# Kernel tuning notes

Hardware: AMD Instinct MI355X
Metric: run time of the kernel (lower is better)

The kernel has to match this reference:

```python
import jax, jax.numpy as jnp
import numpy as np

N, IN_SIZE, FEAT, N_OUT = 8192, 512, 128, 512
ALPHA = 0.5


def setup_inputs() -> dict:
    key = jax.random.key(0)
    ks = jax.random.split(key, 5)
    return {
        "x": jax.random.normal(ks[0], (N, IN_SIZE), dtype=jnp.float32),
        "W0": jax.random.normal(ks[1], (FEAT, IN_SIZE), dtype=jnp.float32) * (1.0 / np.sqrt(IN_SIZE)),
        "W1": jax.random.normal(ks[2], (FEAT, IN_SIZE), dtype=jnp.float32) * (1.0 / np.sqrt(IN_SIZE)),
        "weight": jax.random.normal(ks[3], (IN_SIZE, N_OUT), dtype=jnp.float32),
        "weight_time": jax.random.normal(ks[4], (IN_SIZE, N_OUT), dtype=jnp.float32),
    }


def time_affinity(n: int) -> jnp.ndarray:
    # Closed form of the numpy roll/triu/flip construction: M[i,j] = n - |i-j|,
    # then rows normalized to sum to 1.
    idx = jnp.arange(n)
    M = (n - jnp.abs(idx[:, None] - idx[None, :])).astype(jnp.float32)
    return M / jnp.sum(M, axis=1, keepdims=True)


def reference(x, W0, W1, weight, weight_time):
    n = x.shape[0]
    q = x @ W0.T                      # [N, FEAT]
    k = x @ W1.T                      # [N, FEAT]
    G = jax.nn.softmax(q @ k.T, axis=1)   # [N, N] learned affinity
    G_time = time_affinity(n)              # [N, N] static affinity
    out = (G @ x) @ weight                 # [N, N_OUT]
    out_time = (G_time @ x) @ weight_time  # [N, N_OUT]
    return ALPHA * out + (1.0 - ALPHA) * out_time
```

## Files before the change

### kernel.cpp

```cpp
#include <hip/hip_runtime.h>
#include <math.h>

#define NN 8192
#define INS 512
#define FEAT 128

typedef unsigned short ush;
typedef short bf16x8 __attribute__((ext_vector_type(8)));
typedef float f32x4 __attribute__((ext_vector_type(4)));

__device__ __forceinline__ ush f2bf(float f) {
    unsigned u = __float_as_uint(f);
    unsigned r = (u + 0x7FFFu + ((u >> 16) & 1u)) >> 16;
    return (ush)r;
}
__device__ __forceinline__ float bf2f(ush h) {
    return __uint_as_float(((unsigned)h) << 16);
}
__device__ __forceinline__ void cp16(const ush* g, ush* l) {
    __builtin_amdgcn_global_load_lds(
        (const __attribute__((address_space(1))) void*)g,
        (__attribute__((address_space(3))) void*)l, 16, 0, 0);
}
__device__ __forceinline__ void split8(float4 f0, float4 f1, uint4& h, uint4& l) {
    float f[8] = {f0.x, f0.y, f0.z, f0.w, f1.x, f1.y, f1.z, f1.w};
    unsigned hu[8], lu[8];
    #pragma unroll
    for (int j = 0; j < 8; ++j) {
        unsigned u = __float_as_uint(f[j]);
        hu[j] = u >> 16;
        float lo = f[j] - __uint_as_float(u & 0xFFFF0000u);
        lu[j] = (unsigned)f2bf(lo);
    }
    h.x = hu[0] | (hu[1] << 16); h.y = hu[2] | (hu[3] << 16);
    h.z = hu[4] | (hu[5] << 16); h.w = hu[6] | (hu[7] << 16);
    l.x = lu[0] | (lu[1] << 16); l.y = lu[2] | (lu[3] << 16);
    l.z = lu[4] | (lu[5] << 16); l.w = lu[6] | (lu[7] << 16);
}


__global__ __launch_bounds__(256) void cast_w01(const float* __restrict__ W0,
                                                const float* __restrict__ W1,
                                                ush* __restrict__ W01h,
                                                ush* __restrict__ W01l) {
    int idx = (blockIdx.x * 256 + threadIdx.x) * 8;
    int r = idx >> 9, c = idx & 511;
    const float* src = (r < 128) ? &W0[r * 512 + c] : &W1[(r - 128) * 512 + c];
    float4 f0 = *(const float4*)src;
    float4 f1 = *(const float4*)(src + 4);
    uint4 h, l;
    split8(f0, f1, h, l);
    *(uint4*)&W01h[idx] = h;
    *(uint4*)&W01l[idx] = l;
}

__global__ __launch_bounds__(256) void cast_wT(const float* __restrict__ wm,
                                               const float* __restrict__ wt,
                                               ush* __restrict__ wmTh, ush* __restrict__ wmTl,
                                               ush* __restrict__ wtTh, ush* __restrict__ wtTl) {
    const float* src = blockIdx.z ? wt : wm;
    ush* oh = blockIdx.z ? wtTh : wmTh;
    ush* ol = blockIdx.z ? wtTl : wmTl;
    __shared__ float T[64][65];
    const int t = threadIdx.x;
    const int k0 = blockIdx.y * 64, n0 = blockIdx.x * 64;
    #pragma unroll
    for (int u = 0; u < 4; ++u) {
        int idx = u * 256 + t;
        int r = idx >> 4, c4 = (idx & 15) * 4;
        *(float4*)&T[r][c4] = *(const float4*)&src[(k0 + r) * 512 + n0 + c4];
    }
    __syncthreads();
    #pragma unroll
    for (int u = 0; u < 4; ++u) {
        int idx = u * 256 + t;
        int a = idx >> 4, b4 = (idx & 15) * 4;
        unsigned hu[4], lu[4];
        #pragma unroll
        for (int j = 0; j < 4; ++j) {
            float f = T[b4 + j][a];
            unsigned uu = __float_as_uint(f);
            hu[j] = uu >> 16;
            lu[j] = (unsigned)f2bf(f - __uint_as_float(uu & 0xFFFF0000u));
        }
        uint2 hp, lp;
        hp.x = hu[0] | (hu[1] << 16); hp.y = hu[2] | (hu[3] << 16);
        lp.x = lu[0] | (lu[1] << 16); lp.y = lu[2] | (lu[3] << 16);
        *(uint2*)&oh[(n0 + a) * 512 + k0 + b4] = hp;
        *(uint2*)&ol[(n0 + a) * 512 + k0 + b4] = lp;
    }
}

__global__ __launch_bounds__(256) void gemm_xv(const float* __restrict__ x,
    const ush* __restrict__ wmTh, const ush* __restrict__ wmTl,
    const ush* __restrict__ wtTh, const ush* __restrict__ wtTl,
    ush* __restrict__ vtg, ush* __restrict__ xtb) {
    const bool isV = (blockIdx.z == 0);
    const ush* Bhg = isV ? wmTh : wtTh;
    const ush* Blg = isV ? wmTl : wtTl;
    __shared__ __align__(16) ush sm[20480];
    ush* Ah = sm;
    ush* Al = sm + 5120;
    ush* Bh = sm + 10240;
    ush* Bl = sm + 15360;
    const int t = threadIdx.x;
    const int lane = t & 63, w = t >> 6;
    const int l15 = lane & 15, g4 = lane >> 4;
    const int m0 = blockIdx.y * 128, n0 = blockIdx.x * 128;
    const int wm0 = (w & 1) * 64, wn0 = (w >> 1) * 64;
    f32x4 acc[4][4];
    #pragma unroll
    for (int mt = 0; mt < 4; ++mt)
        #pragma unroll
        for (int nt = 0; nt < 4; ++nt)
            acc[mt][nt] = (f32x4){0.f, 0.f, 0.f, 0.f};

    const int am = t >> 1, akh = (t & 1) * 16;
    for (int k0 = 0; k0 < 512; k0 += 32) {
        __syncthreads();
        {
            const float* src = &x[(m0 + am) * 512 + k0 + akh];
            float4 f0 = *(const float4*)&src[0];
            float4 f1 = *(const float4*)&src[4];
            float4 f2 = *(const float4*)&src[8];
            float4 f3 = *(const float4*)&src[12];
            uint4 h0, l0, h1, l1;
            split8(f0, f1, h0, l0);
            split8(f2, f3, h1, l1);
            int s0 = am * 5 + (akh >> 3);
            *(uint4*)&Ah[s0 * 8] = h0; *(uint4*)&Ah[(s0 + 1) * 8] = h1;
            *(uint4*)&Al[s0 * 8] = l0; *(uint4*)&Al[(s0 + 1) * 8] = l1;
        }
        #pragma unroll
        for (int u = 0; u < 2; ++u) {
            int s = u * 256 + t;
            int n = s >> 2, g = s & 3;
            int srco = (n0 + n) * 512 + k0 + g * 8;
            int slot = n * 5 + g;
            *(uint4*)&Bh[slot * 8] = *(const uint4*)&Bhg[srco];
            *(uint4*)&Bl[slot * 8] = *(const uint4*)&Blg[srco];
        }
        __syncthreads();
        bf16x8 ah[4], al[4], bh[4], bl[4];
        #pragma unroll
        for (int mt = 0; mt < 4; ++mt) {
            int slot = (wm0 + mt * 16 + l15) * 5 + g4;
            ah[mt] = *(const bf16x8*)&Ah[slot * 8];
            al[mt] = *(const bf16x8*)&Al[slot * 8];
        }
        #pragma unroll
        for (int nt = 0; nt < 4; ++nt) {
            int slot = (wn0 + nt * 16 + l15) * 5 + g4;
            bh[nt] = *(const bf16x8*)&Bh[slot * 8];
            bl[nt] = *(const bf16x8*)&Bl[slot * 8];
        }
        #pragma unroll
        for (int mt = 0; mt < 4; ++mt)
            #pragma unroll
            for (int nt = 0; nt < 4; ++nt) {
                acc[mt][nt] = __builtin_amdgcn_mfma_f32_16x16x32_bf16(ah[mt], bh[nt], acc[mt][nt], 0, 0, 0);
                acc[mt][nt] = __builtin_amdgcn_mfma_f32_16x16x32_bf16(al[mt], bh[nt], acc[mt][nt], 0, 0, 0);
                acc[mt][nt] = __builtin_amdgcn_mfma_f32_16x16x32_bf16(ah[mt], bl[nt], acc[mt][nt], 0, 0, 0);
            }
    }

    if (!isV) {
        #pragma unroll
        for (int mt = 0; mt < 4; ++mt)
            #pragma unroll
            for (int nt = 0; nt < 4; ++nt) {
                int col = n0 + wn0 + nt * 16 + l15;
                int rowb = m0 + wm0 + mt * 16 + g4 * 4;
                #pragma unroll
                for (int reg = 0; reg < 4; ++reg)
                    xtb[(rowb + reg) * 512 + col] = f2bf(acc[mt][nt][reg]);
            }
    } else {
        __syncthreads();
        #pragma unroll
        for (int mt = 0; mt < 4; ++mt)
            #pragma unroll
            for (int nt = 0; nt < 4; ++nt) {
                int nl = wn0 + nt * 16 + l15;
                int mb = wm0 + mt * 16 + g4 * 4;
                uint2 pk;
                pk.x = (unsigned)f2bf(acc[mt][nt][0]) | ((unsigned)f2bf(acc[mt][nt][1]) << 16);
                pk.y = (unsigned)f2bf(acc[mt][nt][2]) | ((unsigned)f2bf(acc[mt][nt][3]) << 16);
                *(uint2*)&sm[nl * 136 + mb] = pk;
            }
        __syncthreads();
        int a = t >> 1, off = (t & 1) * 64;
        #pragma unroll
        for (int u = 0; u < 8; ++u)
            *(uint4*)&vtg[(n0 + a) * 8192 + m0 + off + u * 8] =
                *(const uint4*)&sm[a * 136 + off + u * 8];
    }
}

__global__ __launch_bounds__(256) void gemm_qk(const float* __restrict__ x,
    const ush* __restrict__ W01h, const ush* __restrict__ W01l,
    ush* __restrict__ qh, ush* __restrict__ ql,
    ush* __restrict__ kh, ush* __restrict__ kl) {
    __shared__ __align__(16) ush sm[15360];
    ush* Ah = sm;
    ush* Al = sm + 2560;
    ush* Bh = sm + 5120;
    ush* Bl = sm + 10240;
    const int t = threadIdx.x;
    const int lane = t & 63, w = t >> 6;
    const int l15 = lane & 15, g4 = lane >> 4;
    const int m0 = blockIdx.y * 64, n0 = blockIdx.x * 128;
    const int wm0 = (w & 1) * 32, wn0 = (w >> 1) * 64;
    f32x4 acc[2][4];
    #pragma unroll
    for (int mt = 0; mt < 2; ++mt)
        #pragma unroll
        for (int nt = 0; nt < 4; ++nt)
            acc[mt][nt] = (f32x4){0.f, 0.f, 0.f, 0.f};

    const int ar = t >> 2, ag = t & 3;
    for (int k0 = 0; k0 < 512; k0 += 32) {
        __syncthreads();
        {
            const float* src = &x[(m0 + ar) * 512 + k0 + ag * 8];
            float4 f0 = *(const float4*)&src[0];
            float4 f1 = *(const float4*)&src[4];
            uint4 h, l;
            split8(f0, f1, h, l);
            int slot = ar * 5 + ag;
            *(uint4*)&Ah[slot * 8] = h;
            *(uint4*)&Al[slot * 8] = l;
        }
        #pragma unroll
        for (int u = 0; u < 2; ++u) {
            int s = u * 256 + t;
            int n = s >> 2, g = s & 3;
            int srco = (n0 + n) * 512 + k0 + g * 8;
            int slot = n * 5 + g;
            *(uint4*)&Bh[slot * 8] = *(const uint4*)&W01h[srco];
            *(uint4*)&Bl[slot * 8] = *(const uint4*)&W01l[srco];
        }
        __syncthreads();
        bf16x8 ah[2], al[2], bh[4], bl[4];
        #pragma unroll
        for (int mt = 0; mt < 2; ++mt) {
            int slot = (wm0 + mt * 16 + l15) * 5 + g4;
            ah[mt] = *(const bf16x8*)&Ah[slot * 8];
            al[mt] = *(const bf16x8*)&Al[slot * 8];
        }
        #pragma unroll
        for (int nt = 0; nt < 4; ++nt) {
            int slot = (wn0 + nt * 16 + l15) * 5 + g4;
            bh[nt] = *(const bf16x8*)&Bh[slot * 8];
            bl[nt] = *(const bf16x8*)&Bl[slot * 8];
        }
        #pragma unroll
        for (int mt = 0; mt < 2; ++mt)
            #pragma unroll
            for (int nt = 0; nt < 4; ++nt) {
                acc[mt][nt] = __builtin_amdgcn_mfma_f32_16x16x32_bf16(ah[mt], bh[nt], acc[mt][nt], 0, 0, 0);
                acc[mt][nt] = __builtin_amdgcn_mfma_f32_16x16x32_bf16(al[mt], bh[nt], acc[mt][nt], 0, 0, 0);
                acc[mt][nt] = __builtin_amdgcn_mfma_f32_16x16x32_bf16(ah[mt], bl[nt], acc[mt][nt], 0, 0, 0);
            }
    }
    ush* oh = (n0 == 0) ? qh : kh;
    ush* ol = (n0 == 0) ? ql : kl;
    #pragma unroll
    for (int mt = 0; mt < 2; ++mt)
        #pragma unroll
        for (int nt = 0; nt < 4; ++nt) {
            int col = wn0 + nt * 16 + l15;
            int rowb = m0 + wm0 + mt * 16 + g4 * 4;
            #pragma unroll
            for (int reg = 0; reg < 4; ++reg) {
                float v = acc[mt][nt][reg];
                unsigned u = __float_as_uint(v);
                ush h = (ush)(u >> 16);
                ush lo = f2bf(v - __uint_as_float(u & 0xFFFF0000u));
                oh[(rowb + reg) * 128 + col] = h;
                ol[(rowb + reg) * 128 + col] = lo;
            }
        }
}

__global__ __launch_bounds__(256) void time_part1(const ush* __restrict__ xtb,
                                                  float* __restrict__ pP,
                                                  float* __restrict__ pQ) {
    int d = blockIdx.x * 256 + threadIdx.x;
    int r0 = blockIdx.y * 128;
    float sp = 0.f, sq = 0.f;
    for (int r = 0; r < 128; ++r) {
        float v = bf2f(xtb[(r0 + r) * 512 + d]);
        sp += v;
        sq += (float)(r0 + r) * v;
    }
    pP[blockIdx.y * 512 + d] = sp;
    pQ[blockIdx.y * 512 + d] = sq;
}

__global__ __launch_bounds__(512) void time_part2(float* __restrict__ pP,
                                                  float* __restrict__ pQ,
                                                  float* __restrict__ Ad,
                                                  float* __restrict__ Qt) {
    int d = threadIdx.x;
    float rp = 0.f, rq = 0.f;
    for (int c = 0; c < 64; ++c) {
        int idx = c * 512 + d;
        float p = pP[idx], qv = pQ[idx];
        pP[idx] = rp; pQ[idx] = rq;
        rp += p; rq += qv;
    }
    Ad[d] = rp; Qt[d] = rq;
}

__global__ __launch_bounds__(256) void time_part3(const ush* __restrict__ xtb,
                                                  const float* __restrict__ pP,
                                                  const float* __restrict__ pQ,
                                                  const float* __restrict__ Ad,
                                                  const float* __restrict__ Qt,
                                                  float* __restrict__ out) {
    int d = blockIdx.x * 256 + threadIdx.x;
    int r0 = blockIdx.y * 128;
    float P = pP[blockIdx.y * 512 + d];
    float Q = pQ[blockIdx.y * 512 + d];
    float A = Ad[d], Qtot = Qt[d];
    for (int r = 0; r < 128; ++r) {
        int i = r0 + r;
        float v = bf2f(xtb[i * 512 + d]);
        P += v;
        float fi = (float)i;
        Q += fi * v;
        float B = 2.f * fi * P - 2.f * Q + Qtot - fi * A;
        int Si = 67108864 - (i * (i + 1)) / 2 - ((8191 - i) * (8192 - i)) / 2;
        float T = (8192.f * A - B) / (float)Si;
        out[i * 512 + d] = 0.5f * T;
    }
}

__global__ __launch_bounds__(256, 2) void pass1(const ush* __restrict__ qhg,
                                                const ush* __restrict__ qlg,
                                                const ush* __restrict__ khg,
                                                const ush* __restrict__ klg,
                                                float* __restrict__ pm,
                                                float* __restrict__ pl) {
    __shared__ __align__(16) ush Kh3[3][32 * 128];
    __shared__ __align__(16) ush Kl3[3][32 * 128];
    __shared__ float sm_[2][128], sl_[2][128];
    const int t = threadIdx.x;
    const int lane = t & 63, w = t >> 6;
    const int rt0 = w & 1, ct = w >> 1;
    const int b = blockIdx.x;
    const int jc = b & 7, ib = b >> 3;
    const int i0 = ib * 128;
    const int jbase = jc * 1024;
    const int l15 = lane & 15, g = lane >> 4;

    bf16x8 Qh[4][4], Ql[4][4];
    #pragma unroll
    for (int rr = 0; rr < 4; ++rr) {
        int qrow = i0 + (rt0 + 2 * rr) * 16 + l15;
        #pragma unroll
        for (int kt = 0; kt < 4; ++kt) {
            Qh[rr][kt] = *(const bf16x8*)&qhg[qrow * 128 + kt * 32 + g * 8];
            Ql[rr][kt] = *(const bf16x8*)&qlg[qrow * 128 + kt * 32 + g * 8];
        }
    }
    float m_run[4][4], l_run[4][4];
    #pragma unroll
    for (int rr = 0; rr < 4; ++rr)
        #pragma unroll
        for (int reg = 0; reg < 4; ++reg) { m_run[rr][reg] = -INFINITY; l_run[rr][reg] = 0.f; }

    auto stageK = [&](ush* KhD, ush* KlD, int j0) {
        #pragma unroll
        for (int u = 0; u < 2; ++u) {
            int s = u * 256 + t;
            int n = s >> 4, gl = (s & 15) ^ (n & 15);
            int src = (j0 + n) * 128 + gl * 8;
            cp16(&khg[src], &KhD[s * 8]);
            cp16(&klg[src], &KlD[s * 8]);
        }
    };

    ush* KhC = Kh3[0]; ush* KlC = Kl3[0];
    ush* KhN = Kh3[1]; ush* KlN = Kl3[1];
    ush* KhP = Kh3[2]; ush* KlP = Kl3[2];

    stageK(KhC, KlC, jbase);
    stageK(KhN, KlN, jbase + 32);
    __syncthreads();

    for (int jt = 0; jt < 32; ++jt) {
        if (jt < 30) stageK(KhP, KlP, jbase + (jt + 2) * 32);

        bf16x8 kbh[4], kbl[4];
        {
            int n = ct * 16 + l15;
            #pragma unroll
            for (int kt = 0; kt < 4; ++kt) {
                int slot = n * 16 + ((kt * 4 + g) ^ (n & 15));
                kbh[kt] = *(const bf16x8*)&KhC[slot * 8];
                kbl[kt] = *(const bf16x8*)&KlC[slot * 8];
            }
        }
        #pragma unroll
        for (int rr = 0; rr < 4; ++rr) {
            f32x4 sa = {0.f, 0.f, 0.f, 0.f};
            f32x4 sb = {0.f, 0.f, 0.f, 0.f};
            f32x4 sc = {0.f, 0.f, 0.f, 0.f};
            #pragma unroll
            for (int kt = 0; kt < 4; ++kt) sa = __builtin_amdgcn_mfma_f32_16x16x32_bf16(Qh[rr][kt], kbh[kt], sa, 0, 0, 0);
            #pragma unroll
            for (int kt = 0; kt < 4; ++kt) sb = __builtin_amdgcn_mfma_f32_16x16x32_bf16(Ql[rr][kt], kbh[kt], sb, 0, 0, 0);
            #pragma unroll
            for (int kt = 0; kt < 4; ++kt) sc = __builtin_amdgcn_mfma_f32_16x16x32_bf16(Qh[rr][kt], kbl[kt], sc, 0, 0, 0);
            #pragma unroll
            for (int reg = 0; reg < 4; ++reg) {
                float s = (sa[reg] + sb[reg]) + sc[reg];
                float mn = fmaxf(m_run[rr][reg], s);
                l_run[rr][reg] = l_run[rr][reg] * __expf(m_run[rr][reg] - mn) + __expf(s - mn);
                m_run[rr][reg] = mn;
            }
        }

        __syncthreads();
        ush* th = KhC; KhC = KhN; KhN = KhP; KhP = th;
        ush* tl = KlC; KlC = KlN; KlN = KlP; KlP = tl;
    }
    #pragma unroll
    for (int st = 1; st < 16; st <<= 1) {
        #pragma unroll
        for (int rr = 0; rr < 4; ++rr)
            #pragma unroll
            for (int reg = 0; reg < 4; ++reg) {
                float mo = __shfl_xor(m_run[rr][reg], st);
                float lo = __shfl_xor(l_run[rr][reg], st);
                float mn = fmaxf(m_run[rr][reg], mo);
                l_run[rr][reg] = l_run[rr][reg] * __expf(m_run[rr][reg] - mn) + lo * __expf(mo - mn);
                m_run[rr][reg] = mn;
            }
    }
    if (l15 == 0) {
        #pragma unroll
        for (int rr = 0; rr < 4; ++rr)
            #pragma unroll
            for (int reg = 0; reg < 4; ++reg) {
                int row = (rt0 + 2 * rr) * 16 + g * 4 + reg;
                sm_[ct][row] = m_run[rr][reg];
                sl_[ct][row] = l_run[rr][reg];
            }
    }
    __syncthreads();
    if (t < 128) {
        float M = fmaxf(sm_[0][t], sm_[1][t]);
        float l = sl_[0][t] * __expf(sm_[0][t] - M) + sl_[1][t] * __expf(sm_[1][t] - M);
        pm[jc * 8192 + i0 + t] = M;
        pl[jc * 8192 + i0 + t] = l;
    }
}

__global__ __launch_bounds__(256) void merge_stats(const float* __restrict__ pm,
                                                   const float* __restrict__ pl,
                                                   float* __restrict__ Mrow,
                                                   float* __restrict__ Rl) {
    int i = blockIdx.x * 256 + threadIdx.x;
    float M = pm[i];
    #pragma unroll
    for (int js = 1; js < 8; ++js) M = fmaxf(M, pm[js * 8192 + i]);
    float l = 0.f;
    #pragma unroll
    for (int js = 0; js < 8; ++js) l += pl[js * 8192 + i] * __expf(pm[js * 8192 + i] - M);
    Mrow[i] = M;
    Rl[i] = 1.0f / l;
}

__global__ __launch_bounds__(512, 2) void pass2(const ush* __restrict__ qhg,
                                                const ush* __restrict__ qlg,
                                                const ush* __restrict__ khg,
                                                const ush* __restrict__ klg,
                                                const ush* __restrict__ vtg,
                                                const float* __restrict__ Mrow,
                                                const float* __restrict__ Rl,
                                                ush* __restrict__ part0,
                                                ush* __restrict__ part1) {
    __shared__ __align__(16) ush Kh3[3][512 * 8];
    __shared__ __align__(16) ush Kl3[3][512 * 8];
    __shared__ __align__(16) ush Pd[2][64 * 40];

    const int t = threadIdx.x;
    const int lane = t & 63, w = t >> 6;
    const int l15 = lane & 15, g = lane >> 4;
    const int rq = w & 3, ch = w >> 2;
    const int b = blockIdx.x;
    const int xcd = b & 7, lid = b >> 3;
    const int jhalf = xcd >> 2;
    const int strip = (xcd & 3) * 32 + lid;
    const int i0 = strip * 64;
    const int jbase = jhalf * 4096;

    bf16x8 Qh[4], Ql[4];
    {
        int qrow = i0 + rq * 16 + l15;
        #pragma unroll
        for (int kt = 0; kt < 4; ++kt) {
            Qh[kt] = *(const bf16x8*)&qhg[qrow * 128 + kt * 32 + g * 8];
            Ql[kt] = *(const bf16x8*)&qlg[qrow * 128 + kt * 32 + g * 8];
        }
    }
    float Mv[4], Rv[4];
    #pragma unroll
    for (int reg = 0; reg < 4; ++reg) {
        int row = i0 + rq * 16 + g * 4 + reg;
        Mv[reg] = Mrow[row];
        Rv[reg] = Rl[row];
    }

    f32x4 acc[4][4];
    #pragma unroll
    for (int mt = 0; mt < 4; ++mt)
        #pragma unroll
        for (int nt = 0; nt < 4; ++nt)
            acc[mt][nt] = (f32x4){0.f, 0.f, 0.f, 0.f};

    const int vbase = w * 64 + l15;
    bf16x8 vf[4];

    auto stageK = [&](ush* KhD, ush* KlD, int j0) {
        int n = t >> 4, gl = (t & 15) ^ (n & 15);
        int src = (j0 + n) * 128 + gl * 8;
        cp16(&khg[src], &KhD[t * 8]);
        cp16(&klg[src], &KlD[t * 8]);
    };
    auto loadV = [&](int j0) {
        #pragma unroll
        for (int mt = 0; mt < 4; ++mt)
            vf[mt] = *(const bf16x8*)&vtg[(vbase + mt * 16) * 8192 + j0 + g * 8];
    };

    ush* KhC = Kh3[0]; ush* KlC = Kl3[0];
    ush* KhN = Kh3[1]; ush* KlN = Kl3[1];
    ush* KhP = Kh3[2]; ush* KlP = Kl3[2];
    ush* Pc = Pd[0];  ush* Po = Pd[1];

    stageK(KhC, KlC, jbase);
    stageK(KhN, KlN, jbase + 32);
    loadV(jbase);
    __syncthreads();

    for (int jt = 0; jt < 128; ++jt) {
        bf16x8 kbh[4], kbl[4];
        {
            int n = ch * 16 + l15;
            #pragma unroll
            for (int kt = 0; kt < 4; ++kt) {
                int slot = n * 16 + ((kt * 4 + g) ^ (n & 15));
                kbh[kt] = *(const bf16x8*)&KhC[slot * 8];
                kbl[kt] = *(const bf16x8*)&KlC[slot * 8];
            }
        }
        f32x4 sa = {0.f, 0.f, 0.f, 0.f};
        f32x4 sb = {0.f, 0.f, 0.f, 0.f};
        f32x4 sc = {0.f, 0.f, 0.f, 0.f};
        #pragma unroll
        for (int kt = 0; kt < 4; ++kt) sa = __builtin_amdgcn_mfma_f32_16x16x32_bf16(Qh[kt], kbh[kt], sa, 0, 0, 0);
        #pragma unroll
        for (int kt = 0; kt < 4; ++kt) sb = __builtin_amdgcn_mfma_f32_16x16x32_bf16(Ql[kt], kbh[kt], sb, 0, 0, 0);
        #pragma unroll
        for (int kt = 0; kt < 4; ++kt) sc = __builtin_amdgcn_mfma_f32_16x16x32_bf16(Qh[kt], kbl[kt], sc, 0, 0, 0);
        #pragma unroll
        for (int reg = 0; reg < 4; ++reg) {
            float s = (sa[reg] + sb[reg]) + sc[reg];
            float p = __expf(s - Mv[reg]) * Rv[reg];
            Pc[(rq * 16 + g * 4 + reg) * 40 + ch * 16 + l15] = f2bf(p);
        }

        __syncthreads();

        bf16x8 Pb[4];
        #pragma unroll
        for (int nt = 0; nt < 4; ++nt)
            Pb[nt] = *(const bf16x8*)&Pc[(nt * 16 + l15) * 40 + g * 8];
        #pragma unroll
        for (int mt = 0; mt < 4; ++mt)
            #pragma unroll
            for (int nt = 0; nt < 4; ++nt)
                acc[mt][nt] = __builtin_amdgcn_mfma_f32_16x16x32_bf16(vf[mt], Pb[nt], acc[mt][nt], 0, 0, 0);

        if (jt < 127) loadV(jbase + (jt + 1) * 32);
        if (jt < 126) stageK(KhP, KlP, jbase + (jt + 2) * 32);

        ush* th = KhC; KhC = KhN; KhN = KhP; KhP = th;
        ush* tl = KlC; KlC = KlN; KlN = KlP; KlP = tl;
        ush* tp = Pc; Pc = Po; Po = tp;
    }

    ush* prt = (jhalf == 0) ? part0 : part1;
    #pragma unroll
    for (int mt = 0; mt < 4; ++mt)
        #pragma unroll
        for (int nt = 0; nt < 4; ++nt) {
            int qrow = i0 + nt * 16 + l15;
            int vcol = w * 64 + mt * 16 + g * 4;
            uint2 pk;
            pk.x = (unsigned)f2bf(acc[mt][nt][0]) | ((unsigned)f2bf(acc[mt][nt][1]) << 16);
            pk.y = (unsigned)f2bf(acc[mt][nt][2]) | ((unsigned)f2bf(acc[mt][nt][3]) << 16);
            *(uint2*)&prt[qrow * 512 + vcol] = pk;
        }
}

__global__ __launch_bounds__(256) void merge_k(const ush* __restrict__ p0,
                                               const ush* __restrict__ p1,
                                               float* __restrict__ out) {
    int base = (blockIdx.x * 256 + threadIdx.x) * 8;
    uint4 a = *(const uint4*)&p0[base];
    uint4 b = *(const uint4*)&p1[base];
    float4 o0 = *(float4*)&out[base];
    float4 o1 = *(float4*)&out[base + 4];
    unsigned av[4] = {a.x, a.y, a.z, a.w};
    unsigned bv[4] = {b.x, b.y, b.z, b.w};
    float r[8];
    #pragma unroll
    for (int i = 0; i < 4; ++i) {
        r[2 * i + 0] = 0.5f * (bf2f((ush)(av[i] & 0xFFFF)) + bf2f((ush)(bv[i] & 0xFFFF)));
        r[2 * i + 1] = 0.5f * (bf2f((ush)(av[i] >> 16)) + bf2f((ush)(bv[i] >> 16)));
    }
    o0.x += r[0]; o0.y += r[1]; o0.z += r[2]; o0.w += r[3];
    o1.x += r[4]; o1.y += r[5]; o1.z += r[6]; o1.w += r[7];
    *(float4*)&out[base] = o0;
    *(float4*)&out[base + 4] = o1;
}

extern "C" void kernel_launch(void* const* d_in, const int* in_sizes, int n_in,
                              void* d_out, int out_size, void* d_ws, size_t ws_size,
                              hipStream_t stream) {
    const float* x  = (const float*)d_in[0];
    const float* W0 = (const float*)d_in[1];
    const float* W1 = (const float*)d_in[2];
    const float* wm = (const float*)d_in[3];
    const float* wt = (const float*)d_in[4];
    float* out = (float*)d_out;
    float* ws  = (float*)d_ws;

    ush* vtg = (ush*)(ws + 0);
    ush* xtb  = (ush*)(ws + 2097152);
    float* Mr = ws + 2097152;
    float* Rl = ws + 2105344;
    float* pm = ws + 2113536;
    float* pl = ws + 2179072;
    ush* W01h = (ush*)(ws + 4194304);
    ush* W01l = (ush*)(ws + 4259840);
    ush* wmTh = (ush*)(ws + 4325376);
    ush* wmTl = (ush*)(ws + 4456448);
    ush* wtTh = (ush*)(ws + 4587520);
    ush* wtTl = (ush*)(ws + 4718592);
    ush* part0 = (ush*)(ws + 4194304);
    ush* part1 = (ush*)(ws + 6291456);
    ush* qh = (ush*)(ws + 8388608);
    ush* ql = (ush*)(ws + 8912896);
    ush* kh = (ush*)(ws + 9437184);
    ush* kl = (ush*)(ws + 9961472);
    float* pP = ws + 10485760;
    float* pQ = ws + 10518528;
    float* Ad = ws + 10551296;
    float* Qt = ws + 10551808;

    cast_w01   <<<dim3(64),       256, 0, stream>>>(W0, W1, W01h, W01l);
    cast_wT    <<<dim3(8, 8, 2),  256, 0, stream>>>(wm, wt, wmTh, wmTl, wtTh, wtTl);
    gemm_xv    <<<dim3(4, 64, 2), 256, 0, stream>>>(x, wmTh, wmTl, wtTh, wtTl, vtg, xtb);
    gemm_qk    <<<dim3(2, 128),   256, 0, stream>>>(x, W01h, W01l, qh, ql, kh, kl);
    time_part1 <<<dim3(2, 64),    256, 0, stream>>>(xtb, pP, pQ);
    time_part2 <<<dim3(1),        512, 0, stream>>>(pP, pQ, Ad, Qt);
    time_part3 <<<dim3(2, 64),    256, 0, stream>>>(xtb, pP, pQ, Ad, Qt, out);
    pass1      <<<dim3(512),      256, 0, stream>>>(qh, ql, kh, kl, pm, pl);
    merge_stats<<<dim3(32),       256, 0, stream>>>(pm, pl, Mr, Rl);
    pass2      <<<dim3(256),      512, 0, stream>>>(qh, ql, kh, kl, vtg, Mr, Rl, part0, part1);
    merge_k    <<<dim3(2048),     256, 0, stream>>>(part0, part1, out);
}
```

Baseline: 375.6 us.

## Warp-specialize pass2 into score and PV warps with LDS-staged V

Splits the eight waves of pass2 into two groups. Four waves compute the QK scores and exp probabilities for the current tile, while the other four run the P·V MFMAs for the previous tile, so the two stages are software-pipelined. V is now staged into swizzled LDS through async global_load_lds copies, replacing per-wave register loads from global memory, and each PV wave accumulates 8x4 tiles. This should overlap exp/score work with PV matrix work, at the cost of more LDS, doubled accumulator registers per PV wave and possible imbalance between the two groups.

```diff
diff --git a/kernel.cpp b/kernel.cpp
--- a/kernel.cpp
+++ b/kernel.cpp
@@ -483,47 +483,46 @@
                                                 const float* __restrict__ Rl,
                                                 ush* __restrict__ part0,
                                                 ush* __restrict__ part1) {
-    __shared__ __align__(16) ush Kh3[3][512 * 8];
-    __shared__ __align__(16) ush Kl3[3][512 * 8];
-    __shared__ __align__(16) ush Pd[2][64 * 40];
+    __shared__ __align__(16) ush Kh0[512 * 8],  Kh1[512 * 8];
+    __shared__ __align__(16) ush Kl0[512 * 8],  Kl1[512 * 8];
+    __shared__ __align__(16) ush Vt0[2048 * 8], Vt1[2048 * 8];
+    __shared__ __align__(16) ush Pd0[64 * 40],  Pd1[64 * 40];
 
     const int t = threadIdx.x;
     const int lane = t & 63, w = t >> 6;
     const int l15 = lane & 15, g = lane >> 4;
-    const int rq = w & 3, ch = w >> 2;
     const int b = blockIdx.x;
     const int xcd = b & 7, lid = b >> 3;
     const int jhalf = xcd >> 2;
     const int strip = (xcd & 3) * 32 + lid;
     const int i0 = strip * 64;
     const int jbase = jhalf * 4096;
+    const bool isS = (w < 4);
+    const int wp = w & 3;
 
     bf16x8 Qh[4], Ql[4];
-    {
-        int qrow = i0 + rq * 16 + l15;
+    float Mv[4], Rv[4];
+    if (isS) {
+        int qrow = i0 + wp * 16 + l15;
         #pragma unroll
         for (int kt = 0; kt < 4; ++kt) {
             Qh[kt] = *(const bf16x8*)&qhg[qrow * 128 + kt * 32 + g * 8];
             Ql[kt] = *(const bf16x8*)&qlg[qrow * 128 + kt * 32 + g * 8];
         }
-    }
-    float Mv[4], Rv[4];
-    #pragma unroll
-    for (int reg = 0; reg < 4; ++reg) {
-        int row = i0 + rq * 16 + g * 4 + reg;
-        Mv[reg] = Mrow[row];
-        Rv[reg] = Rl[row];
-    }
-
-    f32x4 acc[4][4];
-    #pragma unroll
-    for (int mt = 0; mt < 4; ++mt)
+        #pragma unroll
+        for (int reg = 0; reg < 4; ++reg) {
+            int row = i0 + wp * 16 + g * 4 + reg;
+            Mv[reg] = Mrow[row];
+            Rv[reg] = Rl[row];
+        }
+    }
+
+    f32x4 acc[8][4];
+    #pragma unroll
+    for (int mt = 0; mt < 8; ++mt)
         #pragma unroll
         for (int nt = 0; nt < 4; ++nt)
             acc[mt][nt] = (f32x4){0.f, 0.f, 0.f, 0.f};
-
-    const int vbase = w * 64 + l15;
-    bf16x8 vf[4];
 
     auto stageK = [&](ush* KhD, ush* KlD, int j0) {
         int n = t >> 4, gl = (t & 15) ^ (n & 15);
@@ -531,81 +530,95 @@
         cp16(&khg[src], &KhD[t * 8]);
         cp16(&klg[src], &KlD[t * 8]);
     };
-    auto loadV = [&](int j0) {
-        #pragma unroll
-        for (int mt = 0; mt < 4; ++mt)
-            vf[mt] = *(const bf16x8*)&vtg[(vbase + mt * 16) * 8192 + j0 + g * 8];
+    auto stageV = [&](ush* VtD, int j0) {
+        #pragma unroll
+        for (int u = 0; u < 4; ++u) {
+            int s = u * 512 + t;
+            int c = s >> 2, gl = (s & 3) ^ ((c >> 1) & 3);
+            cp16(&vtg[c * 8192 + j0 + gl * 8], &VtD[s * 8]);
+        }
     };
-
-    ush* KhC = Kh3[0]; ush* KlC = Kl3[0];
-    ush* KhN = Kh3[1]; ush* KlN = Kl3[1];
-    ush* KhP = Kh3[2]; ush* KlP = Kl3[2];
-    ush* Pc = Pd[0];  ush* Po = Pd[1];
-
-    stageK(KhC, KlC, jbase);
-    stageK(KhN, KlN, jbase + 32);
-    loadV(jbase);
+    auto pvStep = [&](const ush* VtR, const ush* Pr) {
+        bf16x8 Pb[4];
+        #pragma unroll
+        for (int nt = 0; nt < 4; ++nt)
+            Pb[nt] = *(const bf16x8*)&Pr[(nt * 16 + l15) * 40 + g * 8];
+        #pragma unroll
+        for (int mt = 0; mt < 8; ++mt) {
+            int c = wp * 128 + mt * 16 + l15;
+            int slot = c * 4 + (g ^ ((c >> 1) & 3));
+            bf16x8 vfr = *(const bf16x8*)&VtR[slot * 8];
+            #pragma unroll
+            for (int nt = 0; nt < 4; ++nt)
+                acc[mt][nt] = __builtin_amdgcn_mfma_f32_16x16x32_bf16(vfr, Pb[nt], acc[mt][nt], 0, 0, 0);
+        }
+    };
+
+    stageK(Kh0, Kl0, jbase);
     __syncthreads();
 
     for (int jt = 0; jt < 128; ++jt) {
-        bf16x8 kbh[4], kbl[4];
-        {
-            int n = ch * 16 + l15;
-            #pragma unroll
-            for (int kt = 0; kt < 4; ++kt) {
-                int slot = n * 16 + ((kt * 4 + g) ^ (n & 15));
-                kbh[kt] = *(const bf16x8*)&KhC[slot * 8];
-                kbl[kt] = *(const bf16x8*)&KlC[slot * 8];
-            }
-        }
-        f32x4 sa = {0.f, 0.f, 0.f, 0.f};
-        f32x4 sb = {0.f, 0.f, 0.f, 0.f};
-        f32x4 sc = {0.f, 0.f, 0.f, 0.f};
-        #pragma unroll
-        for (int kt = 0; kt < 4; ++kt) sa = __builtin_amdgcn_mfma_f32_16x16x32_bf16(Qh[kt], kbh[kt], sa, 0, 0, 0);
-        #pragma unroll
-        for (int kt = 0; kt < 4; ++kt) sb = __builtin_amdgcn_mfma_f32_16x16x32_bf16(Ql[kt], kbh[kt], sb, 0, 0, 0);
-        #pragma unroll
-        for (int kt = 0; kt < 4; ++kt) sc = __builtin_amdgcn_mfma_f32_16x16x32_bf16(Qh[kt], kbl[kt], sc, 0, 0, 0);
-        #pragma unroll
-        for (int reg = 0; reg < 4; ++reg) {
-            float s = (sa[reg] + sb[reg]) + sc[reg];
-            float p = __expf(s - Mv[reg]) * Rv[reg];
-            Pc[(rq * 16 + g * 4 + reg) * 40 + ch * 16 + l15] = f2bf(p);
-        }
-
-        __syncthreads();
-
-        bf16x8 Pb[4];
-        #pragma unroll
-        for (int nt = 0; nt < 4; ++nt)
-            Pb[nt] = *(const bf16x8*)&Pc[(nt * 16 + l15) * 40 + g * 8];
-        #pragma unroll
-        for (int mt = 0; mt < 4; ++mt)
-            #pragma unroll
-            for (int nt = 0; nt < 4; ++nt)
-                acc[mt][nt] = __builtin_amdgcn_mfma_f32_16x16x32_bf16(vf[mt], Pb[nt], acc[mt][nt], 0, 0, 0);
-
-        if (jt < 127) loadV(jbase + (jt + 1) * 32);
-        if (jt < 126) stageK(KhP, KlP, jbase + (jt + 2) * 32);
-
-        ush* th = KhC; KhC = KhN; KhN = KhP; KhP = th;
-        ush* tl = KlC; KlC = KlN; KlN = KlP; KlP = tl;
-        ush* tp = Pc; Pc = Po; Po = tp;
-    }
-
-    ush* prt = (jhalf == 0) ? part0 : part1;
-    #pragma unroll
-    for (int mt = 0; mt < 4; ++mt)
-        #pragma unroll
-        for (int nt = 0; nt < 4; ++nt) {
-            int qrow = i0 + nt * 16 + l15;
-            int vcol = w * 64 + mt * 16 + g * 4;
-            uint2 pk;
-            pk.x = (unsigned)f2bf(acc[mt][nt][0]) | ((unsigned)f2bf(acc[mt][nt][1]) << 16);
-            pk.y = (unsigned)f2bf(acc[mt][nt][2]) | ((unsigned)f2bf(acc[mt][nt][3]) << 16);
-            *(uint2*)&prt[qrow * 512 + vcol] = pk;
-        }
+        ush* KhC = (jt & 1) ? Kh1 : Kh0;
+        ush* KlC = (jt & 1) ? Kl1 : Kl0;
+        ush* KhN = (jt & 1) ? Kh0 : Kh1;
+        ush* KlN = (jt & 1) ? Kl0 : Kl1;
+        ush* VtW = (jt & 1) ? Vt1 : Vt0;
+        ush* VtR = (jt & 1) ? Vt0 : Vt1;
+        ush* Pw  = (jt & 1) ? Pd1 : Pd0;
+        ush* Pr  = (jt & 1) ? Pd0 : Pd1;
+
+        stageV(VtW, jbase + jt * 32);
+        if (jt < 127) stageK(KhN, KlN, jbase + (jt + 1) * 32);
+
+        if (isS) {
+            #pragma unroll
+            for (int kh = 0; kh < 2; ++kh) {
+                bf16x8 kbh[4], kbl[4];
+                int n = kh * 16 + l15;
+                #pragma unroll
+                for (int kt = 0; kt < 4; ++kt) {
+                    int slot = n * 16 + ((kt * 4 + g) ^ (n & 15));
+                    kbh[kt] = *(const bf16x8*)&KhC[slot * 8];
+                    kbl[kt] = *(const bf16x8*)&KlC[slot * 8];
+                }
+                f32x4 sa = {0.f, 0.f, 0.f, 0.f};
+                f32x4 sb = {0.f, 0.f, 0.f, 0.f};
+                f32x4 sc = {0.f, 0.f, 0.f, 0.f};
+                #pragma unroll
+                for (int kt = 0; kt < 4; ++kt) sa = __builtin_amdgcn_mfma_f32_16x16x32_bf16(Qh[kt], kbh[kt], sa, 0, 0, 0);
+                #pragma unroll
+                for (int kt = 0; kt < 4; ++kt) sb = __builtin_amdgcn_mfma_f32_16x16x32_bf16(Ql[kt], kbh[kt], sb, 0, 0, 0);
+                #pragma unroll
+                for (int kt = 0; kt < 4; ++kt) sc = __builtin_amdgcn_mfma_f32_16x16x32_bf16(Qh[kt], kbl[kt], sc, 0, 0, 0);
+                #pragma unroll
+                for (int reg = 0; reg < 4; ++reg) {
+                    float s = (sa[reg] + sb[reg]) + sc[reg];
+                    float p = __expf(s - Mv[reg]) * Rv[reg];
+                    Pw[(wp * 16 + g * 4 + reg) * 40 + kh * 16 + l15] = f2bf(p);
+                }
+            }
+        } else if (jt > 0) {
+            pvStep(VtR, Pr);
+        }
+        __syncthreads();
+    }
+
+    if (!isS) {
+        pvStep(Vt1, Pd1);
+
+        ush* prt = (jhalf == 0) ? part0 : part1;
+        #pragma unroll
+        for (int mt = 0; mt < 8; ++mt)
+            #pragma unroll
+            for (int nt = 0; nt < 4; ++nt) {
+                int qrow = i0 + nt * 16 + l15;
+                int vcol = wp * 128 + mt * 16 + g * 4;
+                uint2 pk;
+                pk.x = (unsigned)f2bf(acc[mt][nt][0]) | ((unsigned)f2bf(acc[mt][nt][1]) << 16);
+                pk.y = (unsigned)f2bf(acc[mt][nt][2]) | ((unsigned)f2bf(acc[mt][nt][3]) << 16);
+                *(uint2*)&prt[qrow * 512 + vcol] = pk;
+            }
+    }
 }
 
 __global__ __launch_bounds__(256) void merge_k(const ush* __restrict__ p0,
```

Result: no change. 374.4 us (-0.3%).
